# Optimization experiments

Hardware: AMD Instinct MI355X
Metric: run time of the kernel (lower is better)

## Reference

```python
import jax, jax.numpy as jnp
import numpy as np

EPS = 1e-5  # torch LayerNorm default eps

def _layernorm(x):
    mu = x.mean(axis=-1, keepdims=True)
    var = x.var(axis=-1, keepdims=True)  # biased, matches torch
    return (x - mu) / jnp.sqrt(var + EPS)

def setup_inputs() -> dict:
    key = jax.random.key(0)
    k1, k2, k3, k4, k5 = jax.random.split(key, 5)
    B, T, E, H = 8, 2048, 512, 8
    d = E // H
    return {
        "input1": jax.random.normal(k1, (B, T, E), dtype=jnp.float32),
        "Wq": jax.random.normal(k2, (H, d), dtype=jnp.float32) * 0.1,
        "Wk": jax.random.normal(k3, (H, d), dtype=jnp.float32) * 0.1,
        "Wv": jax.random.normal(k4, (H, d, d), dtype=jnp.float32) * 0.1,
        "Wm": jax.random.normal(k5, (E, E), dtype=jnp.float32) * 0.05,
    }

def reference(input1, Wq, Wk, Wv, Wm):
    B, T, E = input1.shape
    H, d = Wq.shape
    xn = _layernorm(input1)                       # norm1 over Embed_Dim
    xh = xn.reshape(B, T, H, d)                   # per-head slices of last dim
    # QLayer surrogates: scalar query/key per token, d-dim value per token
    Q = jnp.einsum('bthd,hd->bht', xh, Wq)        # [B,H,T]
    K = jnp.einsum('bthd,hd->bht', xh, Wk)        # [B,H,T]
    V = jnp.einsum('bthd,hde->bhte', xh, Wv)      # [B,H,T,d]
    # distance attention: A = -(Q_i - K_j)^2
    A = -(Q[:, :, :, None] - K[:, :, None, :]) ** 2   # [B,H,T,T]
    P = jax.nn.softmax(A / (d ** 0.5), axis=-1)
    O = jnp.einsum('bhts,bhse->bhte', P, V)       # [B,H,T,d]
    head_result = O.transpose(0, 2, 1, 3).reshape(B, T, E)  # concat heads
    return head_result @ Wm + input1              # merger + residual
```

## Files before the change

kernel.cpp:

```cpp
#include <hip/hip_runtime.h>

typedef __bf16 bf16x8 __attribute__((ext_vector_type(8)));
typedef short short8 __attribute__((ext_vector_type(8)));
typedef float f32x4 __attribute__((ext_vector_type(4)));

#define TT 2048
#define EE 512
#define NH 8
#define DD 64

#define QSCALE 0.36067376022224085f
#define CSCALE 0.18033688011112042f

__device__ __forceinline__ ushort f2bf(float f) {
  union { float f; unsigned u; } a; a.f = f;
  unsigned u = a.u;
  return (ushort)((u + 0x7FFFu + ((u >> 16) & 1u)) >> 16);
}

__global__ __launch_bounds__(256) void k_ln(
    const float* __restrict__ x, const float* __restrict__ Wq,
    const float* __restrict__ Wk,
    float* __restrict__ Q, float* __restrict__ K, ushort* __restrict__ xnb) {
  const int token = blockIdx.x * 4 + (threadIdx.x >> 6);
  const int l = threadIdx.x & 63;
  const float* xr = x + (size_t)token * EE + l * 8;
  float4 a = *(const float4*)xr;
  float4 c = *(const float4*)(xr + 4);
  float xv[8] = {a.x, a.y, a.z, a.w, c.x, c.y, c.z, c.w};
  float s = 0.f, s2 = 0.f;
#pragma unroll
  for (int i = 0; i < 8; i++) { s += xv[i]; s2 = fmaf(xv[i], xv[i], s2); }
#pragma unroll
  for (int o = 32; o; o >>= 1) { s += __shfl_xor(s, o); s2 += __shfl_xor(s2, o); }
  const float mean = s * (1.f / 512.f);
  const float var = s2 * (1.f / 512.f) - mean * mean;
  const float rstd = rsqrtf(var + 1e-5f);

  float xn[8];
  short8 ob;
#pragma unroll
  for (int i = 0; i < 8; i++) {
    xn[i] = (xv[i] - mean) * rstd;
    ob[i] = (short)f2bf(xn[i]);
  }
  *(short8*)(xnb + (size_t)token * EE + l * 8) = ob;

  const float* wq = Wq + l * 8;
  const float* wk = Wk + l * 8;
  float4 q1 = *(const float4*)wq, q2 = *(const float4*)(wq + 4);
  float4 k1 = *(const float4*)wk, k2 = *(const float4*)(wk + 4);
  float wqv[8] = {q1.x, q1.y, q1.z, q1.w, q2.x, q2.y, q2.z, q2.w};
  float wkv[8] = {k1.x, k1.y, k1.z, k1.w, k2.x, k2.y, k2.z, k2.w};
  float q = 0.f, k = 0.f;
#pragma unroll
  for (int i = 0; i < 8; i++) { q = fmaf(xn[i], wqv[i], q); k = fmaf(xn[i], wkv[i], k); }
#pragma unroll
  for (int o = 4; o; o >>= 1) { q += __shfl_xor(q, o); k += __shfl_xor(k, o); }
  if ((l & 7) == 0) {
    const int h = l >> 3;
    const int b = token >> 11, t = token & (TT - 1);
    const int bh = b * NH + h;
    Q[bh * TT + t] = q * QSCALE;
    K[bh * TT + t] = k;
  }
}

__global__ __launch_bounds__(256) void k_wvm(
    const float* __restrict__ Wv, const float* __restrict__ Wm,
    ushort* __restrict__ Wvmt) {
  const int n = blockIdx.x;
  const int tid = threadIdx.x;
  const int k0 = tid, k1 = tid + 256;
  const int h0 = k0 >> 6, h1 = k1 >> 6;
  float acc0 = 0.f, acc1 = 0.f;
#pragma unroll 8
  for (int e = 0; e < 64; e++) {
    acc0 = fmaf(Wv[k0 * 64 + e], Wm[(h0 * 64 + e) * EE + n], acc0);
    acc1 = fmaf(Wv[k1 * 64 + e], Wm[(h1 * 64 + e) * EE + n], acc1);
  }
  Wvmt[n * EE + k0] = f2bf(acc0);
  Wvmt[n * EE + k1] = f2bf(acc1);
}

__global__ __launch_bounds__(256, 2) void k_attn(
    const float* __restrict__ Q, const float* __restrict__ K,
    const ushort* __restrict__ xnb, ushort* __restrict__ hr) {
  const int sw = (blockIdx.x & 7) * 64 + (blockIdx.x >> 3);
  const int bh = sw >> 3;
  const int q0 = (sw & 7) * 256;
  const int b = bh >> 3, h = bh & 7;
  const int tid = threadIdx.x;
  const int w = tid >> 6, l = tid & 63;
  const int l16 = l & 15, lhi = l >> 4;

  __shared__ float ks[TT];
  __shared__ float cs[TT];
  __shared__ float qs[256];
  __shared__ ushort vt[2][64 * 72];

  const float* Kb = K + bh * TT;
#pragma unroll
  for (int i = 0; i < 8; i++) {
    float kv = Kb[tid + i * 256];
    ks[tid + i * 256] = kv;
    cs[tid + i * 256] = -kv * kv * CSCALE;
  }
  qs[tid] = Q[bh * TT + q0 + tid];

  const ushort* Xb = xnb + (size_t)(b * TT) * EE + h * DD;
  const int j0 = (tid >> 3) * 2;
  const int e0 = (tid & 7) * 8;
  const int offc = ((j0 * 2) ^ ((tid & 7) << 4)) >> 1;

  union u16x8 { uint4 v; ushort u[8]; };
  {
    u16x8 a0, a1;
    const ushort* src = Xb + (size_t)j0 * EE + e0;
    a0.v = *(const uint4*)src;
    a1.v = *(const uint4*)(src + EE);
#pragma unroll
    for (int i = 0; i < 8; i++) {
      unsigned pack = (unsigned)a0.u[i] | ((unsigned)a1.u[i] << 16);
      *(unsigned*)&vt[0][(e0 + i) * 72 + offc] = pack;
    }
  }
  __syncthreads();

  float qv[4];
#pragma unroll
  for (int f = 0; f < 4; f++) qv[f] = qs[w * 64 + f * 16 + l16];

  f32x4 acc[4][4];
  f32x4 accd[4];
#pragma unroll
  for (int f = 0; f < 4; f++) {
    accd[f] = (f32x4){0.f, 0.f, 0.f, 0.f};
#pragma unroll
    for (int c = 0; c < 4; c++) acc[f][c] = (f32x4){0.f, 0.f, 0.f, 0.f};
  }
  short8 onesbits = {0x3F80, 0x3F80, 0x3F80, 0x3F80, 0x3F80, 0x3F80, 0x3F80, 0x3F80};
  const bf16x8 ones = __builtin_bit_cast(bf16x8, onesbits);

  int p = 0;
  for (int jt = 0; jt < TT; jt += 64) {
    u16x8 b0, b1;
    const bool more = (jt + 64) < TT;
    if (more) {
      const ushort* srcn = Xb + (size_t)(jt + 64 + j0) * EE + e0;
      b0.v = *(const uint4*)srcn;
      b1.v = *(const uint4*)(srcn + EE);
    }

    __builtin_amdgcn_s_setprio(1);
#pragma unroll
    for (int kk = 0; kk < 2; kk++) {
      bf16x8 vf[4];
#pragma unroll
      for (int c = 0; c < 4; c++) {
        int e = c * 16 + l16;
        int offb = ((kk * 64 + lhi * 16) ^ (((e >> 3) & 7) << 4)) >> 1;
        vf[c] = *(const bf16x8*)&vt[p][e * 72 + offb];
      }
      const int jb = jt + kk * 32 + lhi * 8;
      float4 ka = *(const float4*)&ks[jb];
      float4 kb = *(const float4*)&ks[jb + 4];
      float4 ca = *(const float4*)&cs[jb];
      float4 cb = *(const float4*)&cs[jb + 4];
      float kv[8] = {ka.x, ka.y, ka.z, ka.w, kb.x, kb.y, kb.z, kb.w};
      float cv[8] = {ca.x, ca.y, ca.z, ca.w, cb.x, cb.y, cb.z, cb.w};
#pragma unroll
      for (int f = 0; f < 4; f++) {
        const float qf = qv[f];
        bf16x8 pa;
#pragma unroll
        for (int i = 0; i < 8; i++) {
          float p2 = __builtin_amdgcn_exp2f(fmaf(qf, kv[i], cv[i]));
          pa[i] = (__bf16)p2;
        }
        accd[f] = __builtin_amdgcn_mfma_f32_16x16x32_bf16(pa, ones, accd[f], 0, 0, 0);
#pragma unroll
        for (int c = 0; c < 4; c++)
          acc[f][c] = __builtin_amdgcn_mfma_f32_16x16x32_bf16(pa, vf[c], acc[f][c], 0, 0, 0);
      }
    }
    __builtin_amdgcn_s_setprio(0);

    if (more) {
#pragma unroll
      for (int i = 0; i < 8; i++) {
        unsigned pack = (unsigned)b0.u[i] | ((unsigned)b1.u[i] << 16);
        *(unsigned*)&vt[p ^ 1][(e0 + i) * 72 + offc] = pack;
      }
    }
    __syncthreads();
    p ^= 1;
  }

#pragma unroll
  for (int f = 0; f < 4; f++) {
#pragma unroll
    for (int r = 0; r < 4; r++) {
      float rinv = 1.f / accd[f][r];
      int qrow = q0 + w * 64 + f * 16 + lhi * 4 + r;
      size_t base = ((size_t)(b * TT + qrow)) * EE + h * DD + l16;
#pragma unroll
      for (int c = 0; c < 4; c++)
        hr[base + c * 16] = f2bf(acc[f][c][r] * rinv);
    }
  }
}

__global__ __launch_bounds__(256, 2) void k_merge(
    const ushort* __restrict__ hr, const ushort* __restrict__ Wmt,
    const float* __restrict__ x, float* __restrict__ out) {
  const int n0 = blockIdx.x * 128;
  const int m0 = blockIdx.y * 128;
  const int tid = threadIdx.x;
  const int w = tid >> 6, l = tid & 63;
  const int l16 = l & 15, lhi = l >> 4;
  const int wm = w >> 1, wn = w & 1;

  __shared__ ushort As[2][128 * 72];
  __shared__ ushort Bs[2][128 * 72];
  f32x4 acc[4][4];
#pragma unroll
  for (int i = 0; i < 4; i++)
#pragma unroll
    for (int j = 0; j < 4; j++) acc[i][j] = (f32x4){0.f, 0.f, 0.f, 0.f};

  const int row = tid >> 1, half = tid & 1;
  const ushort* sa0 = hr + (size_t)(m0 + row) * EE + half * 32;
  const ushort* sb0 = Wmt + (size_t)(n0 + row) * EE + half * 32;

  {
    uint4* da = (uint4*)&As[0][row * 72 + half * 32];
    uint4* db = (uint4*)&Bs[0][row * 72 + half * 32];
#pragma unroll
    for (int i = 0; i < 4; i++) da[i] = *(const uint4*)(sa0 + i * 8);
#pragma unroll
    for (int i = 0; i < 4; i++) db[i] = *(const uint4*)(sb0 + i * 8);
  }
  __syncthreads();

  int p = 0;
  for (int k0 = 0; k0 < EE; k0 += 64) {
    const bool more = (k0 + 64) < EE;
    uint4 pa[4], pb[4];
    if (more) {
#pragma unroll
      for (int i = 0; i < 4; i++) pa[i] = *(const uint4*)(sa0 + k0 + 64 + i * 8);
#pragma unroll
      for (int i = 0; i < 4; i++) pb[i] = *(const uint4*)(sb0 + k0 + 64 + i * 8);
    }
#pragma unroll
    for (int kk = 0; kk < 2; kk++) {
      bf16x8 af[4], bfr[4];
#pragma unroll
      for (int mi = 0; mi < 4; mi++)
        af[mi] = *(const bf16x8*)&As[p][(wm * 64 + mi * 16 + l16) * 72 + kk * 32 + lhi * 8];
#pragma unroll
      for (int ni = 0; ni < 4; ni++)
        bfr[ni] = *(const bf16x8*)&Bs[p][(wn * 64 + ni * 16 + l16) * 72 + kk * 32 + lhi * 8];
#pragma unroll
      for (int mi = 0; mi < 4; mi++)
#pragma unroll
        for (int ni = 0; ni < 4; ni++)
          acc[mi][ni] = __builtin_amdgcn_mfma_f32_16x16x32_bf16(af[mi], bfr[ni], acc[mi][ni], 0, 0, 0);
    }
    if (more) {
      uint4* da = (uint4*)&As[p ^ 1][row * 72 + half * 32];
      uint4* db = (uint4*)&Bs[p ^ 1][row * 72 + half * 32];
#pragma unroll
      for (int i = 0; i < 4; i++) da[i] = pa[i];
#pragma unroll
      for (int i = 0; i < 4; i++) db[i] = pb[i];
    }
    __syncthreads();
    p ^= 1;
  }

#pragma unroll
  for (int mi = 0; mi < 4; mi++) {
#pragma unroll
    for (int r = 0; r < 4; r++) {
      const int grow = m0 + wm * 64 + mi * 16 + lhi * 4 + r;
#pragma unroll
      for (int ni = 0; ni < 4; ni++) {
        const int gcol = n0 + wn * 64 + ni * 16 + l16;
        size_t idx = (size_t)grow * EE + gcol;
        out[idx] = acc[mi][ni][r] + x[idx];
      }
    }
  }
}

extern "C" void kernel_launch(void* const* d_in, const int* in_sizes, int n_in,
                              void* d_out, int out_size, void* d_ws, size_t ws_size,
                              hipStream_t stream) {
  const float* x  = (const float*)d_in[0];
  const float* Wq = (const float*)d_in[1];
  const float* Wk = (const float*)d_in[2];
  const float* Wv = (const float*)d_in[3];
  const float* Wm = (const float*)d_in[4];
  float* out = (float*)d_out;

  char* ws = (char*)d_ws;
  float*  Qp   = (float*)(ws);
  float*  Kp   = (float*)(ws + 524288);
  ushort* xnb  = (ushort*)(ws + 1048576);
  ushort* hrp  = (ushort*)(ws + 17825792);
  ushort* Wvmt = (ushort*)(ws + 34603008);

  k_ln<<<4096, 256, 0, stream>>>(x, Wq, Wk, Qp, Kp, xnb);
  k_wvm<<<EE, 256, 0, stream>>>(Wv, Wm, Wvmt);
  k_attn<<<512, 256, 0, stream>>>(Qp, Kp, xnb, hrp);
  k_merge<<<dim3(EE / 128, (8 * TT) / 128), 256, 0, stream>>>(hrp, Wvmt, x, out);
}
```

Before: 127.8 us.

## Pre-transpose V into per-head transposed layout and load MFMA fragments directly

Adds a transpose kernel that writes the normalized activations as [bh][d][T] so the attention kernel can load bf16 B-operand fragments straight from global memory into registers. The shared-memory V staging, swizzled writes and per-tile barriers are replaced by register double-buffering of fragments across 64-key tiles. The hr buffer now reuses xnb's workspace region. This adds an extra kernel launch and a full read/write pass over the activations, and raises register pressure in the attention kernel.

```diff
diff --git a/kernel.cpp b/kernel.cpp
--- a/kernel.cpp
+++ b/kernel.cpp
@@ -63,6 +63,35 @@
     const int bh = b * NH + h;
     Q[bh * TT + t] = q * QSCALE;
     K[bh * TT + t] = k;
+  }
+}
+
+__global__ __launch_bounds__(256) void k_tr(const ushort* __restrict__ xnb,
+                                            ushort* __restrict__ xnt) {
+  const int bh = blockIdx.y;
+  const int b = bh >> 3, h = bh & 7;
+  const int t0 = blockIdx.x * 64;
+  const int tid = threadIdx.x;
+  __shared__ ushort tile[64][72];
+
+  {
+    const int i = tid >> 3, ec = (tid & 7) * 8;
+    const ushort* src = xnb + (size_t)(b * TT + t0 + i) * EE + h * DD + ec;
+    *(uint4*)&tile[i][ec] = *(const uint4*)src;
+    *(uint4*)&tile[i + 32][ec] = *(const uint4*)(src + 32 * EE);
+  }
+  __syncthreads();
+  {
+    const int e = tid >> 3, tc = (tid & 7) * 8;
+    union { uint4 v; ushort u[8]; } o0, o1;
+#pragma unroll
+    for (int i = 0; i < 8; i++) {
+      o0.u[i] = tile[tc + i][e];
+      o1.u[i] = tile[tc + i][e + 32];
+    }
+    ushort* dst = xnt + (size_t)(bh * DD + e) * TT + t0 + tc;
+    *(uint4*)dst = o0.v;
+    *(uint4*)(dst + 32 * TT) = o1.v;
   }
 }
 
@@ -85,7 +114,7 @@
 
 __global__ __launch_bounds__(256, 2) void k_attn(
     const float* __restrict__ Q, const float* __restrict__ K,
-    const ushort* __restrict__ xnb, ushort* __restrict__ hr) {
+    const ushort* __restrict__ xnt, ushort* __restrict__ hr) {
   const int sw = (blockIdx.x & 7) * 64 + (blockIdx.x >> 3);
   const int bh = sw >> 3;
   const int q0 = (sw & 7) * 256;
@@ -96,8 +125,6 @@
 
   __shared__ float ks[TT];
   __shared__ float cs[TT];
-  __shared__ float qs[256];
-  __shared__ ushort vt[2][64 * 72];
 
   const float* Kb = K + bh * TT;
 #pragma unroll
@@ -106,30 +133,11 @@
     ks[tid + i * 256] = kv;
     cs[tid + i * 256] = -kv * kv * CSCALE;
   }
-  qs[tid] = Q[bh * TT + q0 + tid];
-
-  const ushort* Xb = xnb + (size_t)(b * TT) * EE + h * DD;
-  const int j0 = (tid >> 3) * 2;
-  const int e0 = (tid & 7) * 8;
-  const int offc = ((j0 * 2) ^ ((tid & 7) << 4)) >> 1;
-
-  union u16x8 { uint4 v; ushort u[8]; };
-  {
-    u16x8 a0, a1;
-    const ushort* src = Xb + (size_t)j0 * EE + e0;
-    a0.v = *(const uint4*)src;
-    a1.v = *(const uint4*)(src + EE);
-#pragma unroll
-    for (int i = 0; i < 8; i++) {
-      unsigned pack = (unsigned)a0.u[i] | ((unsigned)a1.u[i] << 16);
-      *(unsigned*)&vt[0][(e0 + i) * 72 + offc] = pack;
-    }
-  }
   __syncthreads();
 
   float qv[4];
 #pragma unroll
-  for (int f = 0; f < 4; f++) qv[f] = qs[w * 64 + f * 16 + l16];
+  for (int f = 0; f < 4; f++) qv[f] = Q[bh * TT + q0 + w * 64 + f * 16 + l16];
 
   f32x4 acc[4][4];
   f32x4 accd[4];
@@ -142,60 +150,51 @@
   short8 onesbits = {0x3F80, 0x3F80, 0x3F80, 0x3F80, 0x3F80, 0x3F80, 0x3F80, 0x3F80};
   const bf16x8 ones = __builtin_bit_cast(bf16x8, onesbits);
 
-  int p = 0;
-  for (int jt = 0; jt < TT; jt += 64) {
-    u16x8 b0, b1;
-    const bool more = (jt + 64) < TT;
-    if (more) {
-      const ushort* srcn = Xb + (size_t)(jt + 64 + j0) * EE + e0;
-      b0.v = *(const uint4*)srcn;
-      b1.v = *(const uint4*)(srcn + EE);
-    }
-
+  const ushort* Xt = xnt + (size_t)bh * (DD * TT) + (size_t)l16 * TT;
+  const int jo = lhi * 8;
+
+  bf16x8 fA[8], fB[8];
+
+#define LOADF(dst, jt_) do {                                                   \
+    _Pragma("unroll") for (int c = 0; c < 4; c++)                              \
+    _Pragma("unroll") for (int kk = 0; kk < 2; kk++)                           \
+      dst[c * 2 + kk] =                                                        \
+          *(const bf16x8*)(Xt + (size_t)c * 16 * TT + (jt_) + kk * 32 + jo);   \
+  } while (0)
+
+#define COMPUTE(fr, jt_) do {                                                  \
+    _Pragma("unroll") for (int kk = 0; kk < 2; kk++) {                         \
+      const int jb = (jt_) + kk * 32 + jo;                                     \
+      float4 ka = *(const float4*)&ks[jb];                                     \
+      float4 kb2 = *(const float4*)&ks[jb + 4];                                \
+      float4 ca = *(const float4*)&cs[jb];                                     \
+      float4 cb2 = *(const float4*)&cs[jb + 4];                                \
+      float kv8[8] = {ka.x, ka.y, ka.z, ka.w, kb2.x, kb2.y, kb2.z, kb2.w};     \
+      float cv8[8] = {ca.x, ca.y, ca.z, ca.w, cb2.x, cb2.y, cb2.z, cb2.w};     \
+      _Pragma("unroll") for (int f = 0; f < 4; f++) {                          \
+        bf16x8 pa;                                                             \
+        _Pragma("unroll") for (int i = 0; i < 8; i++)                          \
+          pa[i] = (__bf16)__builtin_amdgcn_exp2f(fmaf(qv[f], kv8[i], cv8[i])); \
+        accd[f] = __builtin_amdgcn_mfma_f32_16x16x32_bf16(pa, ones, accd[f], 0, 0, 0); \
+        _Pragma("unroll") for (int c = 0; c < 4; c++)                          \
+          acc[f][c] = __builtin_amdgcn_mfma_f32_16x16x32_bf16(pa, fr[c * 2 + kk], acc[f][c], 0, 0, 0); \
+      }                                                                        \
+    }                                                                          \
+  } while (0)
+
+  LOADF(fA, 0);
+  for (int jt = 0; jt < TT; jt += 128) {
+    LOADF(fB, jt + 64);
     __builtin_amdgcn_s_setprio(1);
-#pragma unroll
-    for (int kk = 0; kk < 2; kk++) {
-      bf16x8 vf[4];
-#pragma unroll
-      for (int c = 0; c < 4; c++) {
-        int e = c * 16 + l16;
-        int offb = ((kk * 64 + lhi * 16) ^ (((e >> 3) & 7) << 4)) >> 1;
-        vf[c] = *(const bf16x8*)&vt[p][e * 72 + offb];
-      }
-      const int jb = jt + kk * 32 + lhi * 8;
-      float4 ka = *(const float4*)&ks[jb];
-      float4 kb = *(const float4*)&ks[jb + 4];
-      float4 ca = *(const float4*)&cs[jb];
-      float4 cb = *(const float4*)&cs[jb + 4];
-      float kv[8] = {ka.x, ka.y, ka.z, ka.w, kb.x, kb.y, kb.z, kb.w};
-      float cv[8] = {ca.x, ca.y, ca.z, ca.w, cb.x, cb.y, cb.z, cb.w};
-#pragma unroll
-      for (int f = 0; f < 4; f++) {
-        const float qf = qv[f];
-        bf16x8 pa;
-#pragma unroll
-        for (int i = 0; i < 8; i++) {
-          float p2 = __builtin_amdgcn_exp2f(fmaf(qf, kv[i], cv[i]));
-          pa[i] = (__bf16)p2;
-        }
-        accd[f] = __builtin_amdgcn_mfma_f32_16x16x32_bf16(pa, ones, accd[f], 0, 0, 0);
-#pragma unroll
-        for (int c = 0; c < 4; c++)
-          acc[f][c] = __builtin_amdgcn_mfma_f32_16x16x32_bf16(pa, vf[c], acc[f][c], 0, 0, 0);
-      }
-    }
+    COMPUTE(fA, jt);
     __builtin_amdgcn_s_setprio(0);
-
-    if (more) {
-#pragma unroll
-      for (int i = 0; i < 8; i++) {
-        unsigned pack = (unsigned)b0.u[i] | ((unsigned)b1.u[i] << 16);
-        *(unsigned*)&vt[p ^ 1][(e0 + i) * 72 + offc] = pack;
-      }
-    }
-    __syncthreads();
-    p ^= 1;
-  }
+    if (jt + 128 < TT) LOADF(fA, jt + 128);
+    __builtin_amdgcn_s_setprio(1);
+    COMPUTE(fB, jt + 64);
+    __builtin_amdgcn_s_setprio(0);
+  }
+#undef LOADF
+#undef COMPUTE
 
 #pragma unroll
   for (int f = 0; f < 4; f++) {
@@ -309,11 +308,13 @@
   float*  Qp   = (float*)(ws);
   float*  Kp   = (float*)(ws + 524288);
   ushort* xnb  = (ushort*)(ws + 1048576);
-  ushort* hrp  = (ushort*)(ws + 17825792);
+  ushort* hrp  = (ushort*)(ws + 1048576);
+  ushort* xnt  = (ushort*)(ws + 17825792);
   ushort* Wvmt = (ushort*)(ws + 34603008);
 
   k_ln<<<4096, 256, 0, stream>>>(x, Wq, Wk, Qp, Kp, xnb);
+  k_tr<<<dim3(TT / 64, 8 * NH), 256, 0, stream>>>(xnb, xnt);
   k_wvm<<<EE, 256, 0, stream>>>(Wv, Wm, Wvmt);
-  k_attn<<<512, 256, 0, stream>>>(Qp, Kp, xnb, hrp);
+  k_attn<<<512, 256, 0, stream>>>(Qp, Kp, xnt, hrp);
   k_merge<<<dim3(EE / 128, (8 * TT) / 128), 256, 0, stream>>>(hrp, Wvmt, x, out);
 }
```

Measured after the change: 145.0 us. 1.13x slower.
